# Optimization experiments

Hardware: AMD Instinct MI355X
Metric: run time of the kernel (lower is better)

## Reference

```python
import jax, jax.numpy as jnp
import numpy as np


def _gcn_conv(x, edge_index_sl, deg_inv_sqrt, W, b, num_nodes):
    """One GCNConv layer (PyG semantics, normalize=True, self-loops already in edge_index_sl)."""
    h = x @ W  # [N, F_out] dense projection first (F_out <= F_in)
    src = edge_index_sl[0]
    dst = edge_index_sl[1]
    norm = deg_inv_sqrt[src] * deg_inv_sqrt[dst]  # [E+N]
    msg = h[src] * norm[:, None]                  # gather + scale
    out = jax.ops.segment_sum(msg, dst, num_segments=num_nodes)  # scatter-add
    return out + b


def _prep_graph(edge_index, num_nodes):
    # GCNConv(normalize=True) adds self-loops, then deg over destination nodes.
    loops = jnp.arange(num_nodes, dtype=edge_index.dtype)
    ei = jnp.concatenate([edge_index, jnp.stack([loops, loops])], axis=1)  # [2, E+N]
    deg = jax.ops.segment_sum(jnp.ones(ei.shape[1], dtype=jnp.float32), ei[1], num_segments=num_nodes)
    deg_inv_sqrt = jnp.where(deg > 0, jax.lax.rsqrt(deg), 0.0)
    return ei, deg_inv_sqrt


def setup_inputs() -> dict:
    key = jax.random.key(0)
    k1, k2, k3, k4 = jax.random.split(key, 4)
    N, E, D_IN, D_H, D_OUT = 100000, 1200000, 128, 64, 1
    x = jax.random.normal(k1, (N, D_IN), dtype=jnp.float32)
    edge_index = jax.random.randint(k2, (2, E), 0, N, dtype=jnp.int64)
    # Glorot-ish init for weights
    W1 = jax.random.normal(k3, (D_IN, D_H), dtype=jnp.float32) * (1.0 / np.sqrt(D_IN))
    b1 = jnp.zeros((D_H,), dtype=jnp.float32)
    W2 = jax.random.normal(k4, (D_H, D_OUT), dtype=jnp.float32) * (1.0 / np.sqrt(D_H))
    b2 = jnp.zeros((D_OUT,), dtype=jnp.float32)
    return {"x": x, "edge_index": edge_index, "W1": W1, "b1": b1, "W2": W2, "b2": b2}


def reference(x, edge_index, W1, b1, W2, b2):
    num_nodes = x.shape[0]
    ei, dinv = _prep_graph(edge_index, num_nodes)
    h = jax.nn.relu(_gcn_conv(x, ei, dinv, W1, b1, num_nodes))
    # F.dropout(training=self.training) is identity in eval mode (reference baseline)
    out = _gcn_conv(h, ei, dinv, W2, b2, num_nodes)
    return out
```

## Files before the change

### kernel.cpp

```cpp
#include <hip/hip_runtime.h>


#define NBLK 256
#define MAXB 8192

__device__ __forceinline__ float bf2f(unsigned short u) {
    union { unsigned int i; float f; } v; v.i = ((unsigned int)u) << 16; return v.f;
}
__device__ __forceinline__ unsigned short f2bf(float f) {
    union { float f; unsigned int i; } v; v.f = f;
    unsigned int r = (v.i + 0x7fffu + ((v.i >> 16) & 1u)) >> 16;
    return (unsigned short)r;
}

__global__ __launch_bounds__(256) void k_hist(const int* __restrict__ dst, int E, int chunk,
                                              int NB, int* __restrict__ bh) {
    __shared__ int h[512];
    int blk = blockIdx.x, t = threadIdx.x;
    h[t] = 0; h[t + 256] = 0;
    __syncthreads();
    int e0 = blk * chunk, e1 = min(E, e0 + chunk);
    for (int e = e0 + t; e < e1; e += 256) atomicAdd(&h[dst[e] >> 8], 1);
    __syncthreads();
    for (int k = t; k < NB; k += 256) bh[blk * NB + k] = h[k];
}

__global__ __launch_bounds__(256) void k_bscan(int* __restrict__ bh, int NB,
                                               int* __restrict__ btot) {
    __shared__ int s[256];
    int k = blockIdx.x, t = threadIdx.x;
    int v = bh[t * NB + k];
    s[t] = v;
    __syncthreads();
    for (int off = 1; off < 256; off <<= 1) {
        int u = (t >= off) ? s[t - off] : 0;
        __syncthreads();
        s[t] += u;
        __syncthreads();
    }
    bh[t * NB + k] = s[t] - v;
    if (t == 255) btot[k] = s[255];
}

__global__ __launch_bounds__(512) void k_cscan(const int* __restrict__ btot, int NB, int E,
                                               int* __restrict__ bbase, int* __restrict__ offs,
                                               int N) {
    __shared__ int s[512];
    int t = threadIdx.x;
    int v = (t < NB) ? btot[t] : 0;
    s[t] = v;
    __syncthreads();
    for (int off = 1; off < 512; off <<= 1) {
        int u = (t >= off) ? s[t - off] : 0;
        __syncthreads();
        s[t] += u;
        __syncthreads();
    }
    if (t < NB) bbase[t] = s[t] - v;
    if (t == 0) offs[N] = E;
}

__global__ __launch_bounds__(256) void k_dscatter(const int* __restrict__ src,
                                                  const int* __restrict__ dst, int E, int chunk,
                                                  const int* __restrict__ bh,
                                                  const int* __restrict__ bbase, int NB,
                                                  unsigned int* __restrict__ grouped) {
    __shared__ int cur[512];
    int blk = blockIdx.x, t = threadIdx.x;
    for (int k = t; k < NB; k += 256) cur[k] = bbase[k] + bh[blk * NB + k];
    __syncthreads();
    int e0 = blk * chunk, e1 = min(E, e0 + chunk);
    for (int e = e0 + t; e < e1; e += 256) {
        int d = dst[e];
        int pos = atomicAdd(&cur[d >> 8], 1);
        grouped[pos] = ((unsigned int)src[e] << 8) | (unsigned int)(d & 255);
    }
}

__global__ __launch_bounds__(256) void k_bfill(const unsigned int* __restrict__ grouped,
                                               const int* __restrict__ bbase,
                                               const int* __restrict__ btot, int N,
                                               int* __restrict__ offs, int* __restrict__ csr,
                                               float* __restrict__ dinv) {
    __shared__ int hist[256], pfx[256], cur[256];
    __shared__ int stage[MAXB];
    int k = blockIdx.x, t = threadIdx.x;
    int base = bbase[k], cnt = btot[k];
    hist[t] = 0;
    __syncthreads();
    for (int i = t; i < cnt; i += 256) atomicAdd(&hist[grouped[base + i] & 255u], 1);
    __syncthreads();
    int v = hist[t];
    pfx[t] = v;
    __syncthreads();
    for (int off = 1; off < 256; off <<= 1) {
        int u = (t >= off) ? pfx[t - off] : 0;
        __syncthreads();
        pfx[t] += u;
        __syncthreads();
    }
    int excl = pfx[t] - v;
    cur[t] = excl;
    int node = (k << 8) + t;
    if (node < N) {
        offs[node] = base + excl;
        dinv[node] = rsqrtf((float)v + 1.0f);
    }
    __syncthreads();
    if (cnt <= MAXB) {
        for (int i = t; i < cnt; i += 256) {
            unsigned int p = grouped[base + i];
            int pos = atomicAdd(&cur[p & 255u], 1);
            stage[pos] = (int)(p >> 8);
        }
        __syncthreads();
        for (int i = t; i < cnt; i += 256) csr[base + i] = stage[i];
    } else {
        for (int i = t; i < cnt; i += 256) {
            unsigned int p = grouped[base + i];
            int pos = atomicAdd(&cur[p & 255u], 1);
            csr[base + pos] = (int)(p >> 8);
        }
    }
}

__global__ __launch_bounds__(256) void k_gemm1(
    const float* __restrict__ x, const float* __restrict__ W1,
    const float* __restrict__ dinv, unsigned short* __restrict__ ppb, int N)
{
    __shared__ float xs[64][132];
    __shared__ float ws[128][64];
    int tid = threadIdx.x;
    int row0 = blockIdx.x * 64;
    {
        const float4* w4 = (const float4*)W1;
        float4* s4 = (float4*)&ws[0][0];
        #pragma unroll
        for (int i = 0; i < 8; i++) s4[tid + 256 * i] = w4[tid + 256 * i];
    }
    {
        int maxr = N - row0; if (maxr > 64) maxr = 64;
        const float4* x4 = (const float4*)(x + (size_t)row0 * 128);
        int n4 = maxr * 32;
        for (int i = tid; i < n4; i += 256) {
            int r = i >> 5, c = i & 31;
            *(float4*)&xs[r][c * 4] = x4[i];
        }
    }
    __syncthreads();
    int c0 = (tid & 15) * 4;
    int r0 = (tid >> 4) * 4;
    float acc[4][4] = {};
    for (int kk = 0; kk < 128; kk += 4) {
        float xv[4][4], wv[4][4];
        #pragma unroll
        for (int i = 0; i < 4; i++) *(float4*)xv[i] = *(const float4*)&xs[r0 + i][kk];
        #pragma unroll
        for (int t = 0; t < 4; t++) *(float4*)wv[t] = *(const float4*)&ws[kk + t][c0];
        #pragma unroll
        for (int i = 0; i < 4; i++)
            #pragma unroll
            for (int j = 0; j < 4; j++)
                acc[i][j] += xv[i][0] * wv[0][j] + xv[i][1] * wv[1][j]
                           + xv[i][2] * wv[2][j] + xv[i][3] * wv[3][j];
    }
    #pragma unroll
    for (int i = 0; i < 4; i++) {
        int r = row0 + r0 + i;
        if (r < N) {
            float d = dinv[r];
            ushort4 o;
            o.x = f2bf(acc[i][0] * d);
            o.y = f2bf(acc[i][1] * d);
            o.z = f2bf(acc[i][2] * d);
            o.w = f2bf(acc[i][3] * d);
            *(ushort4*)&ppb[(size_t)r * 64 + c0] = o;
        }
    }
}

__global__ void k_fused1(const int* __restrict__ offs, const int* __restrict__ csr,
                         const unsigned short* __restrict__ ppb,
                         const float* __restrict__ dinv, const float* __restrict__ b1,
                         const float* __restrict__ W2, float* __restrict__ qp, int N) {
    int t = blockIdx.x * blockDim.x + threadIdx.x;
    int lane = t & 63;
    int half = lane >> 5;
    int hl = lane & 31;
    int node = t >> 6;
    int nstride = (gridDim.x * blockDim.x) >> 6;
    float w2a = W2[2 * hl], w2b = W2[2 * hl + 1];
    float ba = b1[2 * hl], bb = b1[2 * hl + 1];
    for (; node < N; node += nstride) {
        int start = offs[node], end = offs[node + 1];
        float acca = 0.0f, accb = 0.0f;
        if (half == 0) {
            unsigned int v = *(const unsigned int*)&ppb[(size_t)node * 64 + 2 * hl];
            acca = bf2f((unsigned short)v);
            accb = bf2f((unsigned short)(v >> 16));
        }
        for (int j0 = start; j0 < end; j0 += 64) {
            int jj = j0 + lane;
            int idx = (jj < end) ? csr[jj] : 0;
            int m = end - j0; if (m > 64) m = 64;
            for (int kk = 0; kk < m; kk += 8) {
                int sidx[4]; bool act[4];
                #pragma unroll
                for (int q = 0; q < 4; q++) {
                    int ka = kk + 2 * q, kb = ka + 1;
                    int kac = (ka < m) ? ka : m - 1;
                    int kbc = (kb < m) ? kb : m - 1;
                    int s0 = __shfl(idx, kac, 64);
                    int s1 = __shfl(idx, kbc, 64);
                    sidx[q] = half ? s1 : s0;
                    act[q] = half ? (kb < m) : (ka < m);
                }
                unsigned int v[4];
                #pragma unroll
                for (int q = 0; q < 4; q++)
                    if (act[q]) v[q] = *(const unsigned int*)&ppb[(size_t)sidx[q] * 64 + 2 * hl];
                #pragma unroll
                for (int q = 0; q < 4; q++)
                    if (act[q]) {
                        acca += bf2f((unsigned short)(v[q] & 0xffffu));
                        accb += bf2f((unsigned short)(v[q] >> 16));
                    }
            }
        }
        acca += __shfl_xor(acca, 32, 64);
        accb += __shfl_xor(accb, 32, 64);
        float di = dinv[node];
        float ha = fmaxf(di * acca + ba, 0.0f);
        float hb = fmaxf(di * accb + bb, 0.0f);
        float v = ha * w2a + hb * w2b;
        #pragma unroll
        for (int mm = 16; mm > 0; mm >>= 1) v += __shfl_xor(v, mm, 64);
        if (lane == 0) qp[node] = v * di;
    }
}

__global__ void k_fused2(const int* __restrict__ offs, const int* __restrict__ csr,
                         const float* __restrict__ qp, const float* __restrict__ dinv,
                         const float* __restrict__ b2, float* __restrict__ out, int N) {
    int i = blockIdx.x * blockDim.x + threadIdx.x;
    if (i < N) {
        int start = offs[i], end = offs[i + 1];
        float s = qp[i];
        for (int j = start; j < end; j++) s += qp[csr[j]];
        out[i] = dinv[i] * s + b2[0];
    }
}

extern "C" void kernel_launch(void* const* d_in, const int* in_sizes, int n_in,
                              void* d_out, int out_size, void* d_ws, size_t ws_size,
                              hipStream_t stream) {
    const float* x  = (const float*)d_in[0];
    const int*   ei = (const int*)d_in[1];
    const float* W1 = (const float*)d_in[2];
    const float* b1 = (const float*)d_in[3];
    const float* W2 = (const float*)d_in[4];
    const float* b2 = (const float*)d_in[5];
    float* out = (float*)d_out;

    int N = in_sizes[0] / 128;
    int E = in_sizes[1] / 2;
    const int* src = ei;
    const int* dst = ei + E;
    int NB = (N + 255) >> 8;
    int chunk = (E + NBLK - 1) / NBLK;

    size_t Np = ((size_t)N + 255) & ~(size_t)255;
    size_t Ep = ((size_t)E + 255) & ~(size_t)255;
    char* w = (char*)d_ws;
    int* bh      = (int*)w;            w += (size_t)NBLK * 512 * 4;
    int* btot    = (int*)w;            w += 512 * 4;
    int* bbase   = (int*)w;            w += 512 * 4;
    unsigned int* grouped = (unsigned int*)w;  w += Ep * 4;
    int* offs    = (int*)w;            w += (Np + 256) * 4;
    int* csr     = (int*)w;            w += Ep * 4;
    float* dinv  = (float*)w;          w += Np * 4;
    unsigned short* ppb = (unsigned short*)w;  w += Np * 64 * 2;
    float* qp    = (float*)w;

    k_hist<<<NBLK, 256, 0, stream>>>(dst, E, chunk, NB, bh);
    k_bscan<<<NB, 256, 0, stream>>>(bh, NB, btot);
    k_cscan<<<1, 512, 0, stream>>>(btot, NB, E, bbase, offs, N);
    k_dscatter<<<NBLK, 256, 0, stream>>>(src, dst, E, chunk, bh, bbase, NB, grouped);
    k_bfill<<<NB, 256, 0, stream>>>(grouped, bbase, btot, N, offs, csr, dinv);
    k_gemm1<<<(N + 63) / 64, 256, 0, stream>>>(x, W1, dinv, ppb, N);
    k_fused1<<<2048, 256, 0, stream>>>(offs, csr, ppb, dinv, b1, W2, qp, N);
    k_fused2<<<(N + 255) / 256, 256, 0, stream>>>(offs, csr, qp, dinv, b2, out, N);
}
```

Measured before the change: 209.7 us.

## Replace FP32 shared-memory GEMM with bf16 MFMA using pre-packed weight fragments

The first-layer projection x@W1 moves from an FP32 register-tiled shared-memory GEMM to bf16 MFMA 16x16x32 instructions. Each wave loads its A fragments straight from global memory and converts them to bf16. A new single-block kernel pre-packs W1 into MFMA B-fragment layout in workspace. This cuts ALU work and shared-memory staging, at the cost of lower input precision (x and W1 rounded to bf16), an extra tiny launch, and scattered 2-byte output stores.

```diff
diff --git a/kernel.cpp b/kernel.cpp
--- a/kernel.cpp
+++ b/kernel.cpp
@@ -3,6 +3,9 @@
 
 #define NBLK 256
 #define MAXB 8192
+
+typedef __attribute__((ext_vector_type(8))) short bf16x8;
+typedef __attribute__((ext_vector_type(4))) float f32x4;
 
 __device__ __forceinline__ float bf2f(unsigned short u) {
     union { unsigned int i; float f; } v; v.i = ((unsigned int)u) << 16; return v.f;
@@ -11,6 +14,19 @@
     union { float f; unsigned int i; } v; v.f = f;
     unsigned int r = (v.i + 0x7fffu + ((v.i >> 16) & 1u)) >> 16;
     return (unsigned short)r;
+}
+
+__global__ __launch_bounds__(256) void k_packB(const float* __restrict__ W1,
+                                               unsigned short* __restrict__ Bfrag) {
+    for (int i = threadIdx.x; i < 8192; i += 256) {
+        int j    = i & 7;
+        int lane = (i >> 3) & 63;
+        int ks   = (i >> 9) & 3;
+        int nt   = i >> 11;
+        int k = ks * 32 + ((lane >> 4) << 3) + j;
+        int n = nt * 16 + (lane & 15);
+        Bfrag[i] = f2bf(W1[k * 64 + n]);
+    }
 }
 
 __global__ __launch_bounds__(256) void k_hist(const int* __restrict__ dst, int E, int chunk,
@@ -124,57 +140,50 @@
     }
 }
 
-__global__ __launch_bounds__(256) void k_gemm1(
-    const float* __restrict__ x, const float* __restrict__ W1,
+__global__ __launch_bounds__(256) void k_gemm1m(
+    const float* __restrict__ x, const unsigned short* __restrict__ Bfrag,
     const float* __restrict__ dinv, unsigned short* __restrict__ ppb, int N)
 {
-    __shared__ float xs[64][132];
-    __shared__ float ws[128][64];
-    int tid = threadIdx.x;
-    int row0 = blockIdx.x * 64;
-    {
-        const float4* w4 = (const float4*)W1;
-        float4* s4 = (float4*)&ws[0][0];
-        #pragma unroll
-        for (int i = 0; i < 8; i++) s4[tid + 256 * i] = w4[tid + 256 * i];
-    }
-    {
-        int maxr = N - row0; if (maxr > 64) maxr = 64;
-        const float4* x4 = (const float4*)(x + (size_t)row0 * 128);
-        int n4 = maxr * 32;
-        for (int i = tid; i < n4; i += 256) {
-            int r = i >> 5, c = i & 31;
-            *(float4*)&xs[r][c * 4] = x4[i];
-        }
-    }
-    __syncthreads();
-    int c0 = (tid & 15) * 4;
-    int r0 = (tid >> 4) * 4;
-    float acc[4][4] = {};
-    for (int kk = 0; kk < 128; kk += 4) {
-        float xv[4][4], wv[4][4];
-        #pragma unroll
-        for (int i = 0; i < 4; i++) *(float4*)xv[i] = *(const float4*)&xs[r0 + i][kk];
-        #pragma unroll
-        for (int t = 0; t < 4; t++) *(float4*)wv[t] = *(const float4*)&ws[kk + t][c0];
-        #pragma unroll
-        for (int i = 0; i < 4; i++)
-            #pragma unroll
-            for (int j = 0; j < 4; j++)
-                acc[i][j] += xv[i][0] * wv[0][j] + xv[i][1] * wv[1][j]
-                           + xv[i][2] * wv[2][j] + xv[i][3] * wv[3][j];
-    }
+    int lane = threadIdx.x & 63;
+    int wid = threadIdx.x >> 6;
+    int r0 = blockIdx.x * 64 + wid * 16;
+    int arow = r0 + (lane & 15);
+    if (arow > N - 1) arow = N - 1;
+    const float* xrow = x + (size_t)arow * 128 + ((lane >> 4) << 3);
+
+    f32x4 acc0 = {0.f, 0.f, 0.f, 0.f};
+    f32x4 acc1 = {0.f, 0.f, 0.f, 0.f};
+    f32x4 acc2 = {0.f, 0.f, 0.f, 0.f};
+    f32x4 acc3 = {0.f, 0.f, 0.f, 0.f};
+
     #pragma unroll
-    for (int i = 0; i < 4; i++) {
-        int r = row0 + r0 + i;
-        if (r < N) {
-            float d = dinv[r];
-            ushort4 o;
-            o.x = f2bf(acc[i][0] * d);
-            o.y = f2bf(acc[i][1] * d);
-            o.z = f2bf(acc[i][2] * d);
-            o.w = f2bf(acc[i][3] * d);
-            *(ushort4*)&ppb[(size_t)r * 64 + c0] = o;
+    for (int ks = 0; ks < 4; ks++) {
+        float4 a0 = *(const float4*)(xrow + ks * 32);
+        float4 a1 = *(const float4*)(xrow + ks * 32 + 4);
+        bf16x8 a;
+        a[0] = (short)f2bf(a0.x); a[1] = (short)f2bf(a0.y);
+        a[2] = (short)f2bf(a0.z); a[3] = (short)f2bf(a0.w);
+        a[4] = (short)f2bf(a1.x); a[5] = (short)f2bf(a1.y);
+        a[6] = (short)f2bf(a1.z); a[7] = (short)f2bf(a1.w);
+        const bf16x8* bp = (const bf16x8*)(Bfrag + (size_t)ks * 64 * 8 + lane * 8);
+        acc0 = __builtin_amdgcn_mfma_f32_16x16x32_bf16(a, bp[0 * 256], acc0, 0, 0, 0);
+        acc1 = __builtin_amdgcn_mfma_f32_16x16x32_bf16(a, bp[1 * 256], acc1, 0, 0, 0);
+        acc2 = __builtin_amdgcn_mfma_f32_16x16x32_bf16(a, bp[2 * 256], acc2, 0, 0, 0);
+        acc3 = __builtin_amdgcn_mfma_f32_16x16x32_bf16(a, bp[3 * 256], acc3, 0, 0, 0);
+    }
+
+    int c = lane & 15;
+    int rbase = r0 + ((lane >> 4) << 2);
+    #pragma unroll
+    for (int j = 0; j < 4; j++) {
+        int row = rbase + j;
+        if (row < N) {
+            float di = dinv[row];
+            unsigned short* p = ppb + (size_t)row * 64 + c;
+            p[0]  = f2bf(acc0[j] * di);
+            p[16] = f2bf(acc1[j] * di);
+            p[32] = f2bf(acc2[j] * di);
+            p[48] = f2bf(acc3[j] * di);
         }
     }
 }
@@ -280,14 +289,16 @@
     int* csr     = (int*)w;            w += Ep * 4;
     float* dinv  = (float*)w;          w += Np * 4;
     unsigned short* ppb = (unsigned short*)w;  w += Np * 64 * 2;
-    float* qp    = (float*)w;
-
+    float* qp    = (float*)w;          w += Np * 4;
+    unsigned short* Bfrag = (unsigned short*)w;
+
+    k_packB<<<1, 256, 0, stream>>>(W1, Bfrag);
     k_hist<<<NBLK, 256, 0, stream>>>(dst, E, chunk, NB, bh);
     k_bscan<<<NB, 256, 0, stream>>>(bh, NB, btot);
     k_cscan<<<1, 512, 0, stream>>>(btot, NB, E, bbase, offs, N);
     k_dscatter<<<NBLK, 256, 0, stream>>>(src, dst, E, chunk, bh, bbase, NB, grouped);
     k_bfill<<<NB, 256, 0, stream>>>(grouped, bbase, btot, N, offs, csr, dinv);
-    k_gemm1<<<(N + 63) / 64, 256, 0, stream>>>(x, W1, dinv, ppb, N);
+    k_gemm1m<<<(N + 63) / 64, 256, 0, stream>>>(x, Bfrag, dinv, ppb, N);
     k_fused1<<<2048, 256, 0, stream>>>(offs, csr, ppb, dinv, b1, W2, qp, N);
     k_fused2<<<(N + 255) / 256, 256, 0, stream>>>(offs, csr, qp, dinv, b2, out, N);
 }
```

Result: faster. 197.5 us (-5.8%).
